# Kernel optimization log

Hardware: AMD Instinct MI355X
Metric: run time of the kernel (lower is better)

Reference implementation:

```python
import jax, jax.numpy as jnp
from jax import lax
import numpy as np

LOGZERO = -(65504.0 ** 2)  # -torch.finfo(float16).min**2


def setup_inputs() -> dict:
    key = jax.random.key(0)
    ks = jax.random.split(key, 5)
    B, T, D, V, CB, Ly = 32, 512, 512, 4096, 30, 4
    x = jax.random.normal(ks[0], (B, T, D), jnp.float32)
    W = jax.random.normal(ks[1], (V, D), jnp.float32) * 0.02
    b = jax.random.normal(ks[2], (V,), jnp.float32) * 0.02
    xl = jnp.full((B,), T, jnp.int32)
    y = jax.random.randint(ks[3], (B, Ly), 1, V)  # partial hypothesis (last token used)
    # unique candidate ids per row (exclude blank=0) to avoid duplicate-scatter ambiguity
    scores = jax.random.uniform(ks[4], (B, V - 1))
    ctc_beam_idx = jnp.argsort(scores, axis=1)[:, :CB] + 1
    return {"x": x, "W": W, "b": b, "xl": xl, "y": y,
            "ctc_beam_idx": ctc_beam_idx, "blank": 0, "eos": V - 1}


def reference(x, W, b, xl, y, ctc_beam_idx, blank, eos):
    B, T, D = x.shape
    V = W.shape[0]
    CB = ctc_beam_idx.shape[1]
    # forward(): Linear + log_softmax  -> (B, T, V)
    logp = jax.nn.log_softmax(jnp.einsum("btd,vd->btv", x, W) + b, axis=-1)
    # preProcess(): lastP[1] = cumsum of blank logprob over time, lastP[0] = logzero
    blank_lp = logp[:, :, blank]                     # (B, T)
    lastP1 = jnp.cumsum(blank_lp, axis=1).T          # (T, B)
    lastP0 = jnp.full((T, B), LOGZERO, logp.dtype)
    lastPsum = jnp.logaddexp(lastP0, lastP1)         # (T, B)
    # cState.select / bState.select -> candidate and blank scores per beam hyp
    Xn = jnp.take_along_axis(logp, ctc_beam_idx[:, None, :], axis=2)  # (B, T, CB)
    Xn = Xn.transpose(1, 0, 2)                                        # (T, B, CB)
    Xb = jnp.broadcast_to(blank_lp.T[:, :, None], Xn.shape)           # (T, B, CB)
    # prefP: lastPsum everywhere, lastP[1] where candidate == last prediction
    same = (y[:, -1][:, None] == ctc_beam_idx)                        # (B, CB)
    prefP = jnp.where(same[None], lastP1[:, :, None], lastPsum[:, :, None])  # (T, B, CB)
    Ly = y.shape[1]
    start = min(Ly, T - 1)
    loop_start = max(start, 1)
    Pn0 = jnp.full((B, CB), LOGZERO, logp.dtype)
    Pb0 = jnp.full((B, CB), LOGZERO, logp.dtype)
    if start == 0:
        Pn0 = Xn[0]
    def step(carry, inp):
        Pn_prev, Pb_prev = carry
        pref_prev, xn_t, xb_t = inp
        Pn = jnp.logaddexp(Pn_prev, pref_prev) + xn_t
        Pb = jnp.logaddexp(Pn_prev, Pb_prev) + xb_t
        return (Pn, Pb), (Pn, Pb)
    _, (Pn_seq, Pb_seq) = lax.scan(
        step, (Pn0, Pb0),
        (prefP[loop_start - 1:T - 1], Xn[loop_start:], Xb[loop_start:]))
    if start == 0:  # prepend the preset t=0 entry
        Pn_seq = jnp.concatenate([Pn0[None], Pn_seq], axis=0)
        Pb_seq = jnp.concatenate([Pb0[None], Pb_seq], axis=0)
    # curP over t in [start, T)
    curP_t = jnp.logaddexp(Pn_seq, Pb_seq)                            # (T-start, B, CB)
    t_idx = jnp.arange(start, T)
    valid = xl[None, :] > t_idx[:, None]                              # (T-start, B)
    curP_t = jnp.where(valid[:, :, None], curP_t, LOGZERO)
    curP = jax.nn.logsumexp(curP_t, axis=0)                           # (B, CB)
    # scatter into vocab; initial self.prefP == 0.0
    finalP = jnp.full((B, V), LOGZERO, curP.dtype)
    finalP = finalP.at[jnp.arange(B)[:, None], ctc_beam_idx].set(curP)
    # eos score: lastPsum at final valid frame only
    ar = jnp.arange(T)
    maskBT = xl[:, None] > ar[None, :]
    mask0 = (xl - 1)[:, None] > ar[None, :]
    lps = jnp.where(maskBT & ~mask0, lastPsum.T, 0.0)                 # (B, T)
    finalP = finalP.at[:, eos].set(jnp.sum(lps, axis=1))
    finalP = finalP.at[:, blank].set(LOGZERO)
    return finalP
```

## Files before the change

kernel.cpp:

```cpp
#include <hip/hip_runtime.h>
#include <hip/hip_fp8.h>

#define LOGZERO -4290774016.0f
#define L2E 1.4426950408889634f
#define LN2 0.6931471805599453f

constexpr int Bb = 32, Tt = 512, Dd = 512, Vv = 4096;
constexpr int BT = Bb * Tt;

typedef __attribute__((ext_vector_type(4)))  float f32x4;
typedef __attribute__((ext_vector_type(16))) float f32x16;
typedef __attribute__((ext_vector_type(4)))  int   i32x4;
typedef __attribute__((ext_vector_type(8)))  int   i32x8;

#define GLOBAL_AS __attribute__((address_space(1)))
#define LDS_AS    __attribute__((address_space(3)))

__device__ __forceinline__ float fexp2(float x) { return __builtin_amdgcn_exp2f(x); }
__device__ __forceinline__ float flog2(float x) { return __builtin_amdgcn_logf(x); }

__device__ __forceinline__ unsigned cvt4_fp8(float4 v, float s) {
#if __has_builtin(__builtin_amdgcn_cvt_pk_fp8_f32)
  int p = __builtin_amdgcn_cvt_pk_fp8_f32(v.x * s, v.y * s, 0, false);
  p = __builtin_amdgcn_cvt_pk_fp8_f32(v.z * s, v.w * s, p, true);
  return (unsigned)p;
#else
  unsigned b0 = __hip_cvt_float_to_fp8(v.x * s, __HIP_SATFINITE, __HIP_E4M3);
  unsigned b1 = __hip_cvt_float_to_fp8(v.y * s, __HIP_SATFINITE, __HIP_E4M3);
  unsigned b2 = __hip_cvt_float_to_fp8(v.z * s, __HIP_SATFINITE, __HIP_E4M3);
  unsigned b3 = __hip_cvt_float_to_fp8(v.w * s, __HIP_SATFINITE, __HIP_E4M3);
  return b0 | (b1 << 8) | (b2 << 16) | (b3 << 24);
#endif
}

__device__ __forceinline__ float lg2add(float a, float b) {
  float mx = fmaxf(a, b);
  float d  = fabsf(a - b);
  return mx + flog2(1.0f + fexp2(-d));
}

__device__ __forceinline__ i32x8 ld2(const unsigned char* p) {
  i32x4 lo = *(const i32x4*)p;
  i32x4 hx = *(const i32x4*)(p + 1024);
  return __builtin_shufflevector(lo, hx, 0, 1, 2, 3, 4, 5, 6, 7);
}

__global__ __launch_bounds__(256) void kPre(const float* __restrict__ x,
                                            const float* __restrict__ W,
                                            unsigned char* __restrict__ Xfp,
                                            unsigned char* __restrict__ Wp) {
  __shared__ unsigned char T[16384];
  const int tid = threadIdx.x, bid = blockIdx.x;
  const bool isX = bid < 512;
  const float* srcF;
  float scale;
  int cb = 0, half = 0;
  if (isX) {
    srcF = x + (size_t)bid * 32 * Dd;
    scale = 1.0f;
  } else {
    int idx = bid - 512;
    cb = idx >> 1; half = idx & 1;
    srcF = W + ((size_t)cb * 64 + half * 32) * Dd;
    scale = 16.0f;
  }

  #pragma unroll
  for (int p = 0; p < 16; ++p) {
    int f = p * 256 + tid;
    int r = f >> 7;
    int cf = f & 127;
    int c = cf >> 2, m = cf & 3;
    float4 v = *(const float4*)(srcF + (size_t)f * 4);
    unsigned o = cvt4_fp8(v, scale);
    *(unsigned*)(T + ((r * 32 + (c ^ r)) * 16 + m * 4)) = o;
  }
  __syncthreads();

  if (isX) {
    unsigned char* dst = Xfp + (size_t)bid * 16384;
    #pragma unroll
    for (int u = 0; u < 4; ++u) {
      int s = u * 256 + tid;
      int r = s & 31, khalf = (s >> 5) & 1, h = (s >> 6) & 1, kb = s >> 7;
      int c = kb * 4 + khalf * 2 + h;
      uint4 o = *(const uint4*)(T + (r * 32 + (c ^ r)) * 16);
      *(uint4*)(dst + (size_t)s * 16) = o;
    }
  } else {
    unsigned char* dst = Wp + (size_t)cb * 32768;
    #pragma unroll
    for (int u = 0; u < 4; ++u) {
      int lsl = u * 256 + tid;
      int r = lsl & 31, khalf = (lsl >> 5) & 1, h = (lsl >> 6) & 1, kb = lsl >> 7;
      int c = kb * 4 + khalf * 2 + h;
      int s = kb * 256 + half * 128 + h * 64 + khalf * 32 + r;
      uint4 o = *(const uint4*)(T + (r * 32 + (c ^ r)) * 16);
      *(uint4*)(dst + (size_t)s * 16) = o;
    }
  }
}

__global__ __launch_bounds__(256, 4) void kA(const unsigned char* __restrict__ Xfp,
                                             const unsigned char* __restrict__ Wp,
                                             const float* __restrict__ bias,
                                             const int* __restrict__ beam,
                                             const int* __restrict__ blankp,
                                             float* __restrict__ Spart,
                                             float* __restrict__ selL,
                                             int CB) {
  __shared__ unsigned char Ald[32768];
  __shared__ float Spw[4][64];
  __shared__ int   selv[31];
  __shared__ float selb[31];

  const int tid = threadIdx.x;
  const int tileN = blockIdx.x & 15;
  const int tileM = blockIdx.x >> 4;
  const int row0 = tileM * 64, col0 = tileN * 256;
  const int bb = row0 >> 9;
  const int lane = tid & 63, w = tid >> 6;
  const int l31 = lane & 31, hi = lane >> 5;

  if (tid < 31) {
    int v = (tid == 0) ? *blankp : beam[bb * CB + tid - 1];
    selv[tid] = v;
    selb[tid] = bias[v];
  }

  const unsigned char* src = Xfp + (size_t)tileM * 32768;
  #pragma unroll
  for (int i = 0; i < 8; ++i) {
    int off = (w * 8 + i) * 1024;
    __builtin_amdgcn_global_load_lds((const GLOBAL_AS void*)(src + off + lane * 16),
                                     (LDS_AS void*)(Ald + off), 16, 0, 0);
  }
  __syncthreads();

  const int colw = col0 + w * 64;
  const int cb = tileN * 4 + w;

  f32x16 acc[2][2];
  #pragma unroll
  for (int ct = 0; ct < 2; ++ct)
    #pragma unroll
    for (int mt = 0; mt < 2; ++mt)
      #pragma unroll
      for (int r = 0; r < 16; ++r) acc[ct][mt][r] = 0.f;

  const unsigned char* wpB = Wp + (size_t)cb * 32768 + lane * 16;
  const unsigned char* aB  = Ald + lane * 16;

  i32x8 bc[2];
  bc[0] = ld2(wpB);
  bc[1] = ld2(wpB + 2048);

  #pragma unroll 1
  for (int kb = 0; kb < 8; ++kb) {
    i32x8 bn[2];
    const int kn = (kb < 7) ? kb + 1 : 7;
    bn[0] = ld2(wpB + kn * 4096);
    bn[1] = ld2(wpB + kn * 4096 + 2048);
    {
      i32x8 af0 = ld2(aB + kb * 2048);
      acc[0][0] = __builtin_amdgcn_mfma_scale_f32_32x32x64_f8f6f4(
          af0, bc[0], acc[0][0], 0, 0, 0, 0x7f7f7f7f, 0, 0x7b7b7b7b);
      acc[1][0] = __builtin_amdgcn_mfma_scale_f32_32x32x64_f8f6f4(
          af0, bc[1], acc[1][0], 0, 0, 0, 0x7f7f7f7f, 0, 0x7b7b7b7b);
    }
    {
      i32x8 af1 = ld2(aB + 16384 + kb * 2048);
      acc[0][1] = __builtin_amdgcn_mfma_scale_f32_32x32x64_f8f6f4(
          af1, bc[0], acc[0][1], 0, 0, 0, 0x7f7f7f7f, 0, 0x7b7b7b7b);
      acc[1][1] = __builtin_amdgcn_mfma_scale_f32_32x32x64_f8f6f4(
          af1, bc[1], acc[1][1], 0, 0, 0, 0x7f7f7f7f, 0, 0x7b7b7b7b);
    }
    bc[0] = bn[0]; bc[1] = bn[1];
  }

  float bvl[2];
  #pragma unroll
  for (int ct = 0; ct < 2; ++ct)
    bvl[ct] = bias[colw + ct * 32 + l31] * L2E;

  #pragma unroll
  for (int mt = 0; mt < 2; ++mt) {
    #pragma unroll
    for (int reg = 0; reg < 16; ++reg) {
      float s = fexp2(acc[0][mt][reg] * L2E + bvl[0]) +
                fexp2(acc[1][mt][reg] * L2E + bvl[1]);
      s += __shfl_xor(s, 1, 64);
      s += __shfl_xor(s, 2, 64);
      s += __shfl_xor(s, 4, 64);
      s += __shfl_xor(s, 8, 64);
      s += __shfl_xor(s, 16, 64);
      if (l31 == 0)
        Spw[w][mt * 32 + (reg & 3) + 8 * (reg >> 2) + 4 * hi] = s;
    }
  }
  __syncthreads();
  if (tid < 64) {
    float p = Spw[0][tid] + Spw[1][tid] + Spw[2][tid] + Spw[3][tid];
    Spart[(size_t)tileN * BT + row0 + tid] = p;
  }

  const int tbase = row0 & 511;
  #pragma unroll 1
  for (int s = 0; s < 31; ++s) {
    const int vsel = __builtin_amdgcn_readfirstlane(selv[s]);
    const int local = vsel - colw;
    if (local >= 0 && local < 32) {
      const float bvs = selb[s];
      if (l31 == local) {
        #pragma unroll
        for (int mt = 0; mt < 2; ++mt)
          #pragma unroll
          for (int reg = 0; reg < 16; ++reg) {
            int t = tbase + mt * 32 + (reg & 3) + 8 * (reg >> 2) + 4 * hi;
            selL[((size_t)bb * Tt + t) * 31 + s] = acc[0][mt][reg] + bvs;
          }
      }
    } else if (local >= 32 && local < 64) {
      const float bvs = selb[s];
      if (l31 == (local & 31)) {
        #pragma unroll
        for (int mt = 0; mt < 2; ++mt)
          #pragma unroll
          for (int reg = 0; reg < 16; ++reg) {
            int t = tbase + mt * 32 + (reg & 3) + 8 * (reg >> 2) + 4 * hi;
            selL[((size_t)bb * Tt + t) * 31 + s] = acc[1][mt][reg] + bvs;
          }
      }
    }
  }
}

__global__ __launch_bounds__(256) void kC(const float* __restrict__ selL,
                                          const float* __restrict__ Spart,
                                          const int* __restrict__ xl,
                                          const int* __restrict__ beam,
                                          const int* __restrict__ blankp,
                                          const int* __restrict__ eosp,
                                          float* __restrict__ out,
                                          int Ly, int CB) {
  __shared__ float sl[Tt * 31];
  __shared__ float lgS[Tt];
  __shared__ float lastP1[Tt];
  const int b = blockIdx.x, tid = threadIdx.x;

  for (int tt = tid; tt < Tt; tt += 256) {
    float s = 0.f;
    #pragma unroll
    for (int n = 0; n < 16; ++n) s += Spart[(size_t)n * BT + b * Tt + tt];
    lgS[tt] = flog2(s);
  }
  __syncthreads();
  for (int i = tid; i < Tt * 31; i += 256) {
    int t = i / 31;
    sl[i] = selL[(size_t)b * Tt * 31 + i] * L2E - lgS[t];
  }
  __syncthreads();

  float* orow = out + (size_t)b * Vv;
  for (int i = tid; i < Vv; i += 256) orow[i] = LOGZERO;

  const int xlb = xl[b];
  float curP = LOGZERO;
  if (tid < 64) {
    const int lane = tid;
    float vloc[8];
    float run = 0.f;
    #pragma unroll
    for (int u = 0; u < 8; ++u) {
      int t = lane * 8 + u;
      float bl = sl[t * 31];
      run += bl;
      vloc[u] = run;
    }
    float inc = run;
    #pragma unroll
    for (int off = 1; off < 64; off <<= 1) {
      float o = __shfl_up(inc, off, 64);
      if (lane >= off) inc += o;
    }
    float excl = inc - run;
    #pragma unroll
    for (int u = 0; u < 8; ++u) lastP1[lane * 8 + u] = vloc[u] + excl;

    const int kk = (lane < CB) ? lane : (CB - 1);
    const float LOG2ZERO = LOGZERO * L2E;
    float Pn = LOG2ZERO, Pb = LOG2ZERO;
    float mrun = -3.0e38f, srun = 0.0f;
    int start = (Ly < Tt - 1) ? Ly : (Tt - 1);
    if (start == 0) {
      Pn = sl[1 + kk];
      float vv = (0 < xlb) ? lg2add(Pn, Pb) : LOG2ZERO;
      float nm = fmaxf(mrun, vv);
      srun = srun * fexp2(mrun - nm) + fexp2(vv - nm);
      mrun = nm;
    }
    int t0 = (start > 1) ? start : 1;
    float xn_c = sl[t0 * 31 + 1 + kk];
    float xb_c = sl[t0 * 31];
    float pf_c = lastP1[t0 - 1];
    #pragma unroll 2
    for (int t = t0; t < Tt; ++t) {
      int tn = (t + 1 < Tt) ? (t + 1) : (Tt - 1);
      float xn_n = sl[tn * 31 + 1 + kk];
      float xb_n = sl[tn * 31];
      float pf_n = lastP1[tn - 1];
      float Pn2 = lg2add(Pn, pf_c) + xn_c;
      float Pb2 = lg2add(Pn, Pb) + xb_c;
      Pn = Pn2; Pb = Pb2;
      float vv = (t < xlb) ? lg2add(Pn, Pb) : LOG2ZERO;
      float nm = fmaxf(mrun, vv);
      srun = srun * fexp2(mrun - nm) + fexp2(vv - nm);
      mrun = nm;
      xn_c = xn_n; xb_c = xb_n; pf_c = pf_n;
    }
    curP = (mrun + flog2(srun)) * LN2;
  }
  __syncthreads();

  if (tid < 64) {
    if (tid < CB) orow[beam[b * CB + tid]] = curP;
  }
  __syncthreads();
  if (tid == 0) {
    float eosv = (xlb >= 1) ? lastP1[xlb - 1] * LN2 : 0.0f;
    orow[*eosp] = eosv;
    orow[*blankp] = LOGZERO;
  }
}

extern "C" void kernel_launch(void* const* d_in, const int* in_sizes, int n_in,
                              void* d_out, int out_size, void* d_ws, size_t ws_size,
                              hipStream_t stream) {
  (void)n_in; (void)out_size; (void)ws_size;
  const float* x    = (const float*)d_in[0];
  const float* W    = (const float*)d_in[1];
  const float* bias = (const float*)d_in[2];
  const int* xl     = (const int*)d_in[3];
  const int* beam   = (const int*)d_in[5];
  const int* blankp = (const int*)d_in[6];
  const int* eosp   = (const int*)d_in[7];
  const int Ly = in_sizes[4] / Bb;
  const int CB = in_sizes[5] / Bb;

  float* Spart = (float*)d_ws;
  float* selL  = (float*)((char*)d_ws + (size_t)0x100000);
  unsigned char* Xfp = (unsigned char*)((char*)d_ws + (size_t)0x400000);
  unsigned char* Wp  = (unsigned char*)((char*)d_ws + (size_t)0xC00000);
  float* outf = (float*)d_out;

  kPre<<<640, 256, 0, stream>>>(x, W, Xfp, Wp);
  kA<<<4096, 256, 0, stream>>>(Xfp, Wp, bias, beam, blankp, Spart, selL, CB);
  kC<<<Bb, 256, 0, stream>>>(selL, Spart, xl, beam, blankp, eosp, outf, Ly, CB);
}
```

Before: 232.9 us.

## Replace shuffle row-sum with swizzled LDS reduction and defer log-normalizer in scan

In the GEMM epilogue, the per-row exp-sum no longer uses five cross-lane shuffles per register. Each lane writes its partial into the reused A-tile LDS buffer with an XOR swizzle, then 64 threads sum the rows with vector LDS reads. In the scan kernel, loading selL into LDS now happens alongside computing lgS, which removes one barrier and the per-element integer divide. The normalizer is subtracted inside the recurrence instead, and the last iteration is peeled to drop the clamp on the prefetch index. This adds an extra barrier before reusing the LDS buffer and puts a few more LDS reads inside the serial loop.

```diff
diff --git a/kernel.cpp b/kernel.cpp
--- a/kernel.cpp
+++ b/kernel.cpp
@@ -110,7 +110,6 @@
                                              float* __restrict__ selL,
                                              int CB) {
   __shared__ unsigned char Ald[32768];
-  __shared__ float Spw[4][64];
   __shared__ int   selv[31];
   __shared__ float selb[31];
 
@@ -178,30 +177,37 @@
     bc[0] = bn[0]; bc[1] = bn[1];
   }
 
+  __syncthreads();
+  float* P = (float*)Ald;
+
   float bvl[2];
   #pragma unroll
   for (int ct = 0; ct < 2; ++ct)
     bvl[ct] = bias[colw + ct * 32 + l31] * L2E;
 
-  #pragma unroll
-  for (int mt = 0; mt < 2; ++mt) {
-    #pragma unroll
-    for (int reg = 0; reg < 16; ++reg) {
-      float s = fexp2(acc[0][mt][reg] * L2E + bvl[0]) +
-                fexp2(acc[1][mt][reg] * L2E + bvl[1]);
-      s += __shfl_xor(s, 1, 64);
-      s += __shfl_xor(s, 2, 64);
-      s += __shfl_xor(s, 4, 64);
-      s += __shfl_xor(s, 8, 64);
-      s += __shfl_xor(s, 16, 64);
-      if (l31 == 0)
-        Spw[w][mt * 32 + (reg & 3) + 8 * (reg >> 2) + 4 * hi] = s;
+  {
+    const int f = w * 32 + l31;
+    const int chunk = f >> 2, elem = f & 3;
+    #pragma unroll
+    for (int mt = 0; mt < 2; ++mt) {
+      #pragma unroll
+      for (int reg = 0; reg < 16; ++reg) {
+        float s = fexp2(acc[0][mt][reg] * L2E + bvl[0]) +
+                  fexp2(acc[1][mt][reg] * L2E + bvl[1]);
+        int r31 = (reg & 3) + 8 * (reg >> 2) + 4 * hi;
+        int row = mt * 32 + r31;
+        P[row * 128 + ((chunk ^ r31) << 2) + elem] = s;
+      }
     }
   }
   __syncthreads();
   if (tid < 64) {
-    float p = Spw[0][tid] + Spw[1][tid] + Spw[2][tid] + Spw[3][tid];
-    Spart[(size_t)tileN * BT + row0 + tid] = p;
+    const int r31 = tid & 31;
+    f32x4 v = {0.f, 0.f, 0.f, 0.f};
+    #pragma unroll
+    for (int i = 0; i < 32; ++i)
+      v += *(const f32x4*)&P[tid * 128 + ((i ^ r31) << 2)];
+    Spart[(size_t)tileN * BT + row0 + tid] = v[0] + v[1] + v[2] + v[3];
   }
 
   const int tbase = row0 & 511;
@@ -246,18 +252,16 @@
   __shared__ float sl[Tt * 31];
   __shared__ float lgS[Tt];
   __shared__ float lastP1[Tt];
+  __shared__ float blankLp[Tt];
   const int b = blockIdx.x, tid = threadIdx.x;
 
+  for (int i = tid; i < Tt * 31; i += 256)
+    sl[i] = selL[(size_t)b * Tt * 31 + i] * L2E;
   for (int tt = tid; tt < Tt; tt += 256) {
     float s = 0.f;
     #pragma unroll
     for (int n = 0; n < 16; ++n) s += Spart[(size_t)n * BT + b * Tt + tt];
     lgS[tt] = flog2(s);
-  }
-  __syncthreads();
-  for (int i = tid; i < Tt * 31; i += 256) {
-    int t = i / 31;
-    sl[i] = selL[(size_t)b * Tt * 31 + i] * L2E - lgS[t];
   }
   __syncthreads();
 
@@ -273,7 +277,8 @@
     #pragma unroll
     for (int u = 0; u < 8; ++u) {
       int t = lane * 8 + u;
-      float bl = sl[t * 31];
+      float bl = sl[t * 31] - lgS[t];
+      blankLp[t] = bl;
       run += bl;
       vloc[u] = run;
     }
@@ -293,30 +298,43 @@
     float mrun = -3.0e38f, srun = 0.0f;
     int start = (Ly < Tt - 1) ? Ly : (Tt - 1);
     if (start == 0) {
-      Pn = sl[1 + kk];
+      Pn = sl[1 + kk] - lgS[0];
       float vv = (0 < xlb) ? lg2add(Pn, Pb) : LOG2ZERO;
       float nm = fmaxf(mrun, vv);
       srun = srun * fexp2(mrun - nm) + fexp2(vv - nm);
       mrun = nm;
     }
     int t0 = (start > 1) ? start : 1;
-    float xn_c = sl[t0 * 31 + 1 + kk];
-    float xb_c = sl[t0 * 31];
+    float sl_c = sl[t0 * 31 + 1 + kk];
+    float lg_c = lgS[t0];
+    float xb_c = blankLp[t0];
     float pf_c = lastP1[t0 - 1];
     #pragma unroll 2
-    for (int t = t0; t < Tt; ++t) {
-      int tn = (t + 1 < Tt) ? (t + 1) : (Tt - 1);
-      float xn_n = sl[tn * 31 + 1 + kk];
-      float xb_n = sl[tn * 31];
-      float pf_n = lastP1[tn - 1];
-      float Pn2 = lg2add(Pn, pf_c) + xn_c;
+    for (int t = t0; t < Tt - 1; ++t) {
+      float sl_n = sl[(t + 1) * 31 + 1 + kk];
+      float lg_n = lgS[t + 1];
+      float xb_n = blankLp[t + 1];
+      float pf_n = lastP1[t];
+      float xn = sl_c - lg_c;
+      float Pn2 = lg2add(Pn, pf_c) + xn;
       float Pb2 = lg2add(Pn, Pb) + xb_c;
       Pn = Pn2; Pb = Pb2;
       float vv = (t < xlb) ? lg2add(Pn, Pb) : LOG2ZERO;
       float nm = fmaxf(mrun, vv);
       srun = srun * fexp2(mrun - nm) + fexp2(vv - nm);
       mrun = nm;
-      xn_c = xn_n; xb_c = xb_n; pf_c = pf_n;
+      sl_c = sl_n; lg_c = lg_n; xb_c = xb_n; pf_c = pf_n;
+    }
+    {
+      const int t = Tt - 1;
+      float xn = sl_c - lg_c;
+      float Pn2 = lg2add(Pn, pf_c) + xn;
+      float Pb2 = lg2add(Pn, Pb) + xb_c;
+      Pn = Pn2; Pb = Pb2;
+      float vv = (t < xlb) ? lg2add(Pn, Pb) : LOG2ZERO;
+      float nm = fmaxf(mrun, vv);
+      srun = srun * fexp2(mrun - nm) + fexp2(vv - nm);
+      mrun = nm;
     }
     curP = (mrun + flog2(srun)) * LN2;
   }
```

Result: faster. 207.1 us (-11.1%).
